# Performance work log

Hardware: AMD Instinct MI355X
Metric: run time of the kernel (lower is better)

## Reference

```python
import jax, jax.numpy as jnp
import numpy as np

EMBED_DIM = 1024
NUM_HEADS = 16
HEAD_DIM = EMBED_DIM // NUM_HEADS


def setup_inputs() -> dict:
    key = jax.random.key(0)
    ks = jax.random.split(key, 9)
    bs, seq_len = 4, 2048
    s = 1.0 / np.sqrt(EMBED_DIM)
    return {
        "x": jax.random.normal(ks[0], (bs, seq_len, EMBED_DIM), jnp.float32),
        "wq": jax.random.uniform(ks[1], (EMBED_DIM, EMBED_DIM), jnp.float32, -s, s),
        "bq": jax.random.uniform(ks[2], (EMBED_DIM,), jnp.float32, -s, s),
        "wk": jax.random.uniform(ks[3], (EMBED_DIM, EMBED_DIM), jnp.float32, -s, s),
        "bk": jax.random.uniform(ks[4], (EMBED_DIM,), jnp.float32, -s, s),
        "wv": jax.random.uniform(ks[5], (EMBED_DIM, EMBED_DIM), jnp.float32, -s, s),
        "bv": jax.random.uniform(ks[6], (EMBED_DIM,), jnp.float32, -s, s),
        "wo": jax.random.uniform(ks[7], (EMBED_DIM, EMBED_DIM), jnp.float32, -s, s),
        "bo": jax.random.uniform(ks[8], (EMBED_DIM,), jnp.float32, -s, s),
    }


def reference(x, wq, bq, wk, bk, wv, bv, wo, bo):
    bs, seq_len, _ = x.shape
    # projections (torch Linear: y = x @ W.T + b; here w stored as [out,in])
    q = x @ wq.T + bq
    k = x @ wk.T + bk
    v = x @ wv.T + bv
    # split heads -> (bs, heads, seq, head_dim)
    def split(t):
        return t.reshape(bs, seq_len, NUM_HEADS, HEAD_DIM).transpose(0, 2, 1, 3)
    q, k, v = split(q), split(k), split(v)
    scale = 1.0 / jnp.sqrt(jnp.asarray(HEAD_DIM, jnp.float32))
    scores = jnp.einsum("bhqd,bhkd->bhqk", q, k) * scale
    attn = jax.nn.softmax(scores, axis=-1)
    out = jnp.einsum("bhqk,bhkd->bhqd", attn, v)
    out = out.transpose(0, 2, 1, 3).reshape(bs, seq_len, EMBED_DIM)
    return out @ wo.T + bo
```

## Files before the change

kernel.cpp:

```cpp
#include <hip/hip_runtime.h>
#include <stdint.h>

#define SEQ 2048
#define BSZ 4
#define NH 16
#define HD 64
#define EMB 1024
#define NT (SEQ / 64)
#define QSCALE 0.1803368801111f

using bf16x8 = __attribute__((ext_vector_type(8))) __bf16;
using u16x8  = __attribute__((ext_vector_type(8))) unsigned short;
using u32x4  = __attribute__((ext_vector_type(4))) uint32_t;
using f32x4  = __attribute__((ext_vector_type(4))) float;
using f32x16 = __attribute__((ext_vector_type(16))) float;

__device__ __forceinline__ float exp2v(float x) { return __builtin_amdgcn_exp2f(x); }

__device__ __forceinline__ unsigned short f2bf(float f) {
    union { float f; uint32_t u; } v; v.f = f;
    uint32_t r = v.u + 0x7fffu + ((v.u >> 16) & 1u);
    return (unsigned short)(r >> 16);
}

__device__ __forceinline__ uint32_t cvtpk(float lo, float hi) {
    uint32_t r;
    asm("v_cvt_pk_bf16_f32 %0, %1, %2" : "=v"(r) : "v"(lo), "v"(hi));
    return r;
}
__device__ __forceinline__ void plswap(uint32_t& a, uint32_t& b) {
    asm volatile("v_permlane32_swap_b32 %0, %1" : "+v"(a), "+v"(b));
}

__device__ __forceinline__ void gload16(void* lds, const void* g) {
    __builtin_amdgcn_global_load_lds(
        (const __attribute__((address_space(1))) void*)g,
        (__attribute__((address_space(3))) void*)lds, 16, 0, 0);
}

__global__ void cast_kernel(const float* __restrict__ s, unsigned short* __restrict__ d, int n) {
    int i = (blockIdx.x * blockDim.x + threadIdx.x) * 4;
    if (i + 3 >= n) {
        for (int j = 0; j < 4 && i + j < n; ++j) d[i + j] = f2bf(s[i + j]);
        return;
    }
    float4 v = *(const float4*)(s + i);
    ushort4 o;
    o.x = f2bf(v.x); o.y = f2bf(v.y); o.z = f2bf(v.z); o.w = f2bf(v.w);
    *(ushort4*)(d + i) = o;
}

template <int MODE>
__global__ __launch_bounds__(256, 2)
void gemm_bt(const unsigned short* __restrict__ A,
             const unsigned short* __restrict__ Bw,
             const float* __restrict__ b0, const float* __restrict__ b1,
             const float* __restrict__ b2,
             void* __restrict__ C0, void* __restrict__ C1, void* __restrict__ C2,
             int M, int N, int Kd) {
    __shared__ unsigned short As[128][64];
    __shared__ unsigned short Bs[128][64];

    const int t    = threadIdx.x;
    const int lane = t & 63;
    const int wid  = t >> 6;
    const int g    = lane >> 4;
    const int lr   = lane & 15;
    const int wm   = wid >> 1, wn = wid & 1;
    const int m0   = blockIdx.x * 128, n0 = blockIdx.y * 128;
    const int srow = lane >> 3;
    const int scol = (lane & 7) * 8;

    f32x4 acc[4][4];
    const f32x4 zero = {0.f, 0.f, 0.f, 0.f};
#pragma unroll
    for (int i = 0; i < 4; ++i)
#pragma unroll
        for (int j = 0; j < 4; ++j) acc[i][j] = zero;

    for (int kt = 0; kt < Kd; kt += 64) {
#pragma unroll
        for (int p = 0; p < 4; ++p) {
            int rowA = wid * 32 + p * 8;
            gload16(&As[rowA][0], A  + (size_t)(m0 + rowA + srow) * Kd + kt + scol);
            gload16(&Bs[rowA][0], Bw + (size_t)(n0 + rowA + srow) * Kd + kt + scol);
        }
        __syncthreads();
#pragma unroll
        for (int ks = 0; ks < 2; ++ks) {
            bf16x8 af[4], bfr[4];
#pragma unroll
            for (int m = 0; m < 4; ++m)
                af[m] = *(const bf16x8*)&As[wm * 64 + m * 16 + lr][ks * 32 + g * 8];
#pragma unroll
            for (int n = 0; n < 4; ++n)
                bfr[n] = *(const bf16x8*)&Bs[wn * 64 + n * 16 + lr][ks * 32 + g * 8];
#pragma unroll
            for (int m = 0; m < 4; ++m)
#pragma unroll
                for (int n = 0; n < 4; ++n)
                    acc[m][n] = __builtin_amdgcn_mfma_f32_16x16x32_bf16(af[m], bfr[n], acc[m][n], 0, 0, 0);
        }
        __syncthreads();
    }

    int seg = MODE == 2 ? (n0 >> 10) : 0;
    if (MODE == 2 && seg == 2) {
        unsigned short* CwT = (unsigned short*)C2;
        int nl = n0 & 1023;
#pragma unroll
        for (int n = 0; n < 4; ++n) {
            int colL = nl + wn * 64 + n * 16 + lr;
            float bv = b2[colL];
#pragma unroll
            for (int m = 0; m < 4; ++m) {
                int rowg = m0 + wm * 64 + m * 16 + g * 4;
                int bb = rowg >> 11, seq = rowg & 2047;
                ushort4 w;
                w.x = f2bf(acc[m][n][0] + bv);
                w.y = f2bf(acc[m][n][1] + bv);
                w.z = f2bf(acc[m][n][2] + bv);
                w.w = f2bf(acc[m][n][3] + bv);
                *(ushort4*)(CwT + ((size_t)(bb * 1024 + colL)) * SEQ + seq) = w;
            }
        }
        return;
    }

    const float* bias;
    unsigned short* Cw = nullptr;
    float* Cf = nullptr;
    float scl = 1.0f;
    int nl;
    if (MODE == 2) {
        bias = seg == 0 ? b0 : b1;
        Cw = (unsigned short*)(seg == 0 ? C0 : C1);
        scl = seg == 0 ? QSCALE : 1.0f;
        nl = n0 & 1023;
    } else {
        bias = b0; Cf = (float*)C0; nl = n0;
    }
#pragma unroll
    for (int n = 0; n < 4; ++n) {
        int colL = nl + wn * 64 + n * 16 + lr;
        float bv = bias[colL];
#pragma unroll
        for (int m = 0; m < 4; ++m) {
            int rowg = m0 + wm * 64 + m * 16 + g * 4;
#pragma unroll
            for (int r = 0; r < 4; ++r) {
                float val = (acc[m][n][r] + bv) * scl;
                if (MODE == 2)
                    Cw[(size_t)(rowg + r) * EMB + colL] = f2bf(val);
                else
                    Cf[(size_t)(rowg + r) * EMB + colL] = val;
            }
        }
    }
}

__global__ __launch_bounds__(512, 4)
void flash_attn(const unsigned short* __restrict__ Q,
                const unsigned short* __restrict__ K,
                const unsigned short* __restrict__ VT,
                unsigned short* __restrict__ O) {
    __shared__ unsigned char KsB[2][64 * 128];
    __shared__ unsigned char VtB[2][64 * 128];

    const int nwg  = gridDim.x * gridDim.y * gridDim.z;
    const int cpx  = nwg >> 3;
    const int bid0 = (blockIdx.z * gridDim.y + blockIdx.y) * gridDim.x + blockIdx.x;
    const int bid  = (bid0 % 8) * cpx + (bid0 / 8);
    const int bx   = bid & (gridDim.x - 1);
    const int h    = (bid >> 3) & 15;
    const int b    = bid >> 7;

    const int t    = threadIdx.x;
    const int wid  = t >> 6;
    const int lane = t & 63;
    const int l31  = lane & 31;
    const int hi   = lane >> 5;
    const int hi16 = hi << 4;
    const int sw   = (l31 & 7) << 4;
    const int qbase = bx * 256 + wid * 32;
    const size_t rowbase = (size_t)b * SEQ;
    const unsigned short* Kh  = K + rowbase * EMB + h * HD;
    const unsigned short* Vth = VT + (size_t)(b * 1024 + h * HD) * SEQ;

    const int grow = t >> 3;
    const int gc16 = (t & 7) ^ (grow & 7);
    const unsigned short* Ksrc0 = Kh  + (size_t)grow * EMB + gc16 * 8;
    const unsigned short* Vsrc0 = Vth + (size_t)grow * SEQ + gc16 * 8;

    bf16x8 qf[4];
#pragma unroll
    for (int db = 0; db < 4; ++db)
        qf[db] = *(const bf16x8*)(Q + (rowbase + qbase + l31) * EMB + h * HD + db * 16 + hi * 8);

    bf16x8 vones;
#pragma unroll
    for (int j = 0; j < 8; ++j) vones[j] = (__bf16)1.0f;

    f32x16 o0, o1, o2;
#pragma unroll
    for (int r = 0; r < 16; ++r) { o0[r] = 0.f; o1[r] = 0.f; o2[r] = 0.f; }
    float me = -1e30f;

    auto issue_tile = [&](int kt) {
        unsigned char* Ks = KsB[kt & 1] + wid * 1024;
        unsigned char* Vt = VtB[kt & 1] + wid * 1024;
        gload16(Ks, Ksrc0 + (size_t)kt * 64 * EMB);
        gload16(Vt, Vsrc0 + kt * 64);
    };
    issue_tile(0);

    for (int kt = 0; kt < NT; ++kt) {
        unsigned char* Ks = KsB[kt & 1];
        unsigned char* Vt = VtB[kt & 1];

        __syncthreads();

        if (kt + 1 < NT) issue_tile(kt + 1);

        f32x16 s0, s1;
#pragma unroll
        for (int r = 0; r < 16; ++r) { s0[r] = 0.f; s1[r] = 0.f; }
        __builtin_amdgcn_s_setprio(1);
#pragma unroll
        for (int db = 0; db < 4; ++db) {
            bf16x8 kf0 = *(const bf16x8*)(Ks + l31 * 128        + ((db * 32 + hi16) ^ sw));
            bf16x8 kf1 = *(const bf16x8*)(Ks + (l31 + 32) * 128 + ((db * 32 + hi16) ^ sw));
            s0 = __builtin_amdgcn_mfma_f32_32x32x16_bf16(kf0, qf[db], s0, 0, 0, 0);
            s1 = __builtin_amdgcn_mfma_f32_32x32x16_bf16(kf1, qf[db], s1, 0, 0, 0);
        }
        __builtin_amdgcn_s_setprio(0);

        float pm = fmaxf(fmaxf(s0[0], s0[1]), s0[2]);
#pragma unroll
        for (int r = 3; r < 15; r += 2) pm = fmaxf(fmaxf(pm, s0[r]), s0[r + 1]);
        pm = fmaxf(pm, s0[15]);
#pragma unroll
        for (int r = 0; r < 16; r += 2) pm = fmaxf(fmaxf(pm, s1[r]), s1[r + 1]);
        pm = fmaxf(pm, __shfl_xor(pm, 32));

        if (!__all(pm - me <= 8.0f)) {
            float mn = fmaxf(me, pm);
            float al = exp2v(me - mn);
            me = mn;
#pragma unroll
            for (int r = 0; r < 16; ++r) {
                int addr = hi16 + (((r & 3) + 8 * (r >> 2)) << 2);
                float ar = __int_as_float(
                    __builtin_amdgcn_ds_bpermute(addr, __float_as_int(al)));
                o0[r] *= ar; o1[r] *= ar; o2[r] *= ar;
            }
        }

        s0 = s0 - me;
        s1 = s1 - me;
#pragma unroll
        for (int r = 0; r < 16; ++r) s0[r] = exp2v(s0[r]);
#pragma unroll
        for (int r = 0; r < 16; ++r) s1[r] = exp2v(s1[r]);

        bf16x8 pa[4];
#pragma unroll
        for (int kb = 0; kb < 2; ++kb) {
            uint32_t dw[8];
#pragma unroll
            for (int i = 0; i < 8; ++i)
                dw[i] = kb == 0 ? cvtpk(s0[2 * i], s0[2 * i + 1])
                                : cvtpk(s1[2 * i], s1[2 * i + 1]);
            plswap(dw[0], dw[2]); plswap(dw[1], dw[3]);
            plswap(dw[4], dw[6]); plswap(dw[5], dw[7]);
            u32x4 w0 = {dw[0], dw[1], dw[2], dw[3]};
            u32x4 w1 = {dw[4], dw[5], dw[6], dw[7]};
            pa[kb * 2]     = __builtin_bit_cast(bf16x8, w0);
            pa[kb * 2 + 1] = __builtin_bit_cast(bf16x8, w1);
        }

        __builtin_amdgcn_s_setprio(1);
#pragma unroll
        for (int kk = 0; kk < 4; ++kk) {
            bf16x8 vf0 = *(const bf16x8*)(Vt + l31 * 128        + ((kk * 32 + hi16) ^ sw));
            bf16x8 vf1 = *(const bf16x8*)(Vt + (l31 + 32) * 128 + ((kk * 32 + hi16) ^ sw));
            o0 = __builtin_amdgcn_mfma_f32_32x32x16_bf16(pa[kk], vf0, o0, 0, 0, 0);
            o1 = __builtin_amdgcn_mfma_f32_32x32x16_bf16(pa[kk], vf1, o1, 0, 0, 0);
            o2 = __builtin_amdgcn_mfma_f32_32x32x16_bf16(pa[kk], vones, o2, 0, 0, 0);
        }
        __builtin_amdgcn_s_setprio(0);
    }

#pragma unroll
    for (int r = 0; r < 16; ++r) {
        float inv = 1.0f / o2[r];
        int q = qbase + (r & 3) + 8 * (r >> 2) + 4 * hi;
        size_t ro = (rowbase + q) * EMB + h * HD;
        O[ro + l31]      = f2bf(o0[r] * inv);
        O[ro + 32 + l31] = f2bf(o1[r] * inv);
    }
}

extern "C" void kernel_launch(void* const* d_in, const int* in_sizes, int n_in,
                              void* d_out, int out_size, void* d_ws, size_t ws_size,
                              hipStream_t stream) {
    const float* x  = (const float*)d_in[0];
    const float* wq = (const float*)d_in[1];
    const float* bq = (const float*)d_in[2];
    const float* wk = (const float*)d_in[3];
    const float* bk = (const float*)d_in[4];
    const float* wv = (const float*)d_in[5];
    const float* bv = (const float*)d_in[6];
    const float* wo = (const float*)d_in[7];
    const float* bo = (const float*)d_in[8];

    char* ws = (char*)d_ws;
    const size_t M = (size_t)BSZ * SEQ;
    unsigned short* xb    = (unsigned short*)ws;
    unsigned short* wqkvb = (unsigned short*)(ws + (size_t)16 * 1024 * 1024);
    unsigned short* wob   = (unsigned short*)(ws + (size_t)22 * 1024 * 1024);
    unsigned short* Qb    = (unsigned short*)(ws + (size_t)24 * 1024 * 1024);
    unsigned short* Kb    = Qb + M * EMB;
    unsigned short* VTb   = Kb + M * EMB;

    const int nX = (int)(M * EMB);
    cast_kernel<<<nX / 1024, 256, 0, stream>>>(x, xb, nX);
    cast_kernel<<<1024, 256, 0, stream>>>(wq, wqkvb,                 EMB * EMB);
    cast_kernel<<<1024, 256, 0, stream>>>(wk, wqkvb + 1024 * 1024,   EMB * EMB);
    cast_kernel<<<1024, 256, 0, stream>>>(wv, wqkvb + 2 * 1024 * 1024, EMB * EMB);
    cast_kernel<<<1024, 256, 0, stream>>>(wo, wob, EMB * EMB);

    gemm_bt<2><<<dim3(64, 24), 256, 0, stream>>>(xb, wqkvb, bq, bk, bv,
                                                 Qb, Kb, VTb, (int)M, 3 * EMB, EMB);

    flash_attn<<<dim3(SEQ / 256, NH, BSZ), 512, 0, stream>>>(Qb, Kb, VTb, xb);

    gemm_bt<0><<<dim3(64, 8), 256, 0, stream>>>(xb, wob, bo, nullptr, nullptr,
                                                d_out, nullptr, nullptr, (int)M, EMB, EMB);
}
```

Before: 204.6 us.

## Software-pipeline flash attention QK and PV with triple buffering; merge weight casts

Restructures the flash attention loop so the QK^T MFMAs for tile kt are issued alongside the PV MFMAs for tile kt-1, with softmax packing afterwards. K/V LDS buffers go from double to triple buffering to hold the extra in-flight tile. This is meant to hide softmax latency behind matrix work. It also merges the four weight cast launches into one kernel using blockIdx.y to cut launch overhead, at the cost of more LDS per block, which could lower occupancy.

New measurement: 203.6 us. About the same (-0.5%).

```diff
diff --git a/kernel.cpp b/kernel.cpp
--- a/kernel.cpp
+++ b/kernel.cpp
@@ -44,6 +44,24 @@
         for (int j = 0; j < 4 && i + j < n; ++j) d[i + j] = f2bf(s[i + j]);
         return;
     }
+    float4 v = *(const float4*)(s + i);
+    ushort4 o;
+    o.x = f2bf(v.x); o.y = f2bf(v.y); o.z = f2bf(v.z); o.w = f2bf(v.w);
+    *(ushort4*)(d + i) = o;
+}
+
+__global__ void cast4_kernel(const float* __restrict__ w0, const float* __restrict__ w1,
+                             const float* __restrict__ w2, const float* __restrict__ w3,
+                             unsigned short* __restrict__ d0, unsigned short* __restrict__ d1,
+                             unsigned short* __restrict__ d2, unsigned short* __restrict__ d3) {
+    const float* s; unsigned short* d;
+    switch (blockIdx.y) {
+        case 0:  s = w0; d = d0; break;
+        case 1:  s = w1; d = d1; break;
+        case 2:  s = w2; d = d2; break;
+        default: s = w3; d = d3; break;
+    }
+    int i = (blockIdx.x * blockDim.x + threadIdx.x) * 4;
     float4 v = *(const float4*)(s + i);
     ushort4 o;
     o.x = f2bf(v.x); o.y = f2bf(v.y); o.z = f2bf(v.z); o.w = f2bf(v.w);
@@ -164,8 +182,8 @@
                 const unsigned short* __restrict__ K,
                 const unsigned short* __restrict__ VT,
                 unsigned short* __restrict__ O) {
-    __shared__ unsigned char KsB[2][64 * 128];
-    __shared__ unsigned char VtB[2][64 * 128];
+    __shared__ unsigned char KsB[3][64 * 128];
+    __shared__ unsigned char VtB[3][64 * 128];
 
     const int nwg  = gridDim.x * gridDim.y * gridDim.z;
     const int cpx  = nwg >> 3;
@@ -206,23 +224,12 @@
     for (int r = 0; r < 16; ++r) { o0[r] = 0.f; o1[r] = 0.f; o2[r] = 0.f; }
     float me = -1e30f;
 
-    auto issue_tile = [&](int kt) {
-        unsigned char* Ks = KsB[kt & 1] + wid * 1024;
-        unsigned char* Vt = VtB[kt & 1] + wid * 1024;
-        gload16(Ks, Ksrc0 + (size_t)kt * 64 * EMB);
-        gload16(Vt, Vsrc0 + kt * 64);
+    auto issue_tile = [&](int kt, int buf) {
+        gload16(KsB[buf] + wid * 1024, Ksrc0 + (size_t)kt * 64 * EMB);
+        gload16(VtB[buf] + wid * 1024, Vsrc0 + kt * 64);
     };
-    issue_tile(0);
-
-    for (int kt = 0; kt < NT; ++kt) {
-        unsigned char* Ks = KsB[kt & 1];
-        unsigned char* Vt = VtB[kt & 1];
-
-        __syncthreads();
-
-        if (kt + 1 < NT) issue_tile(kt + 1);
-
-        f32x16 s0, s1;
+
+    auto qk = [&](const unsigned char* Ks, f32x16& s0, f32x16& s1) {
 #pragma unroll
         for (int r = 0; r < 16; ++r) { s0[r] = 0.f; s1[r] = 0.f; }
         __builtin_amdgcn_s_setprio(1);
@@ -234,7 +241,22 @@
             s1 = __builtin_amdgcn_mfma_f32_32x32x16_bf16(kf1, qf[db], s1, 0, 0, 0);
         }
         __builtin_amdgcn_s_setprio(0);
-
+    };
+
+    auto pv = [&](const unsigned char* Vt, const bf16x8* pa) {
+        __builtin_amdgcn_s_setprio(1);
+#pragma unroll
+        for (int kk = 0; kk < 4; ++kk) {
+            bf16x8 vf0 = *(const bf16x8*)(Vt + l31 * 128        + ((kk * 32 + hi16) ^ sw));
+            bf16x8 vf1 = *(const bf16x8*)(Vt + (l31 + 32) * 128 + ((kk * 32 + hi16) ^ sw));
+            o0 = __builtin_amdgcn_mfma_f32_32x32x16_bf16(pa[kk], vf0, o0, 0, 0, 0);
+            o1 = __builtin_amdgcn_mfma_f32_32x32x16_bf16(pa[kk], vf1, o1, 0, 0, 0);
+            o2 = __builtin_amdgcn_mfma_f32_32x32x16_bf16(pa[kk], vones, o2, 0, 0, 0);
+        }
+        __builtin_amdgcn_s_setprio(0);
+    };
+
+    auto softmax_pack = [&](f32x16& s0, f32x16& s1, bf16x8* pa, bool first) {
         float pm = fmaxf(fmaxf(s0[0], s0[1]), s0[2]);
 #pragma unroll
         for (int r = 3; r < 15; r += 2) pm = fmaxf(fmaxf(pm, s0[r]), s0[r + 1]);
@@ -243,7 +265,9 @@
         for (int r = 0; r < 16; r += 2) pm = fmaxf(fmaxf(pm, s1[r]), s1[r + 1]);
         pm = fmaxf(pm, __shfl_xor(pm, 32));
 
-        if (!__all(pm - me <= 8.0f)) {
+        if (first) {
+            me = pm;
+        } else if (!__all(pm - me <= 8.0f)) {
             float mn = fmaxf(me, pm);
             float al = exp2v(me - mn);
             me = mn;
@@ -263,7 +287,6 @@
 #pragma unroll
         for (int r = 0; r < 16; ++r) s1[r] = exp2v(s1[r]);
 
-        bf16x8 pa[4];
 #pragma unroll
         for (int kb = 0; kb < 2; ++kb) {
             uint32_t dw[8];
@@ -278,18 +301,29 @@
             pa[kb * 2]     = __builtin_bit_cast(bf16x8, w0);
             pa[kb * 2 + 1] = __builtin_bit_cast(bf16x8, w1);
         }
-
-        __builtin_amdgcn_s_setprio(1);
-#pragma unroll
-        for (int kk = 0; kk < 4; ++kk) {
-            bf16x8 vf0 = *(const bf16x8*)(Vt + l31 * 128        + ((kk * 32 + hi16) ^ sw));
-            bf16x8 vf1 = *(const bf16x8*)(Vt + (l31 + 32) * 128 + ((kk * 32 + hi16) ^ sw));
-            o0 = __builtin_amdgcn_mfma_f32_32x32x16_bf16(pa[kk], vf0, o0, 0, 0, 0);
-            o1 = __builtin_amdgcn_mfma_f32_32x32x16_bf16(pa[kk], vf1, o1, 0, 0, 0);
-            o2 = __builtin_amdgcn_mfma_f32_32x32x16_bf16(pa[kk], vones, o2, 0, 0, 0);
-        }
-        __builtin_amdgcn_s_setprio(0);
-    }
+    };
+
+    issue_tile(0, 0);
+    __syncthreads();
+    issue_tile(1, 1);
+    bf16x8 paA[4];
+    {
+        f32x16 s0, s1;
+        qk(KsB[0], s0, s1);
+        softmax_pack(s0, s1, paA, true);
+    }
+
+    int prv = 0, cur = 1, nxt = 2;
+    for (int kt = 1; kt < NT; ++kt) {
+        __syncthreads();
+        if (kt + 1 < NT) issue_tile(kt + 1, nxt);
+        f32x16 s0, s1;
+        qk(KsB[cur], s0, s1);
+        pv(VtB[prv], paA);
+        softmax_pack(s0, s1, paA, false);
+        int tmp = prv; prv = cur; cur = nxt; nxt = tmp;
+    }
+    pv(VtB[prv], paA);
 
 #pragma unroll
     for (int r = 0; r < 16; ++r) {
@@ -325,10 +359,9 @@
 
     const int nX = (int)(M * EMB);
     cast_kernel<<<nX / 1024, 256, 0, stream>>>(x, xb, nX);
-    cast_kernel<<<1024, 256, 0, stream>>>(wq, wqkvb,                 EMB * EMB);
-    cast_kernel<<<1024, 256, 0, stream>>>(wk, wqkvb + 1024 * 1024,   EMB * EMB);
-    cast_kernel<<<1024, 256, 0, stream>>>(wv, wqkvb + 2 * 1024 * 1024, EMB * EMB);
-    cast_kernel<<<1024, 256, 0, stream>>>(wo, wob, EMB * EMB);
+    cast4_kernel<<<dim3(1024, 4), 256, 0, stream>>>(
+        wq, wk, wv, wo,
+        wqkvb, wqkvb + 1024 * 1024, wqkvb + 2 * 1024 * 1024, wob);
 
     gemm_bt<2><<<dim3(64, 24), 256, 0, stream>>>(xb, wqkvb, bq, bk, bv,
                                                  Qb, Kb, VTb, (int)M, 3 * EMB, EMB);
```

## Process two query sub-tiles per wave in flash attention and merge weight casts

Applied to the files above, without the earlier changes.

Each wave in the flash attention kernel now handles 64 query rows as two 32-row sub-tiles. It reuses the K fragments loaded from LDS and the V fragments across both, while the block drops from 512 to 256 threads. The goal is fewer LDS reads per MFMA and less barrier overhead per unit of work, at the cost of more registers, since there are now six accumulators and two sets of Q fragments, which may lower occupancy. Separately, the four weight-cast launches are merged into one kernel that uses a 2D grid to cut launch overhead.

Measured after the change: 231.7 us. 1.13x slower.

```diff
diff --git a/kernel.cpp b/kernel.cpp
--- a/kernel.cpp
+++ b/kernel.cpp
@@ -44,6 +44,24 @@
         for (int j = 0; j < 4 && i + j < n; ++j) d[i + j] = f2bf(s[i + j]);
         return;
     }
+    float4 v = *(const float4*)(s + i);
+    ushort4 o;
+    o.x = f2bf(v.x); o.y = f2bf(v.y); o.z = f2bf(v.z); o.w = f2bf(v.w);
+    *(ushort4*)(d + i) = o;
+}
+
+__global__ void cast4_kernel(const float* __restrict__ w0, const float* __restrict__ w1,
+                             const float* __restrict__ w2, const float* __restrict__ w3,
+                             unsigned short* __restrict__ d0, unsigned short* __restrict__ d1,
+                             unsigned short* __restrict__ d2, unsigned short* __restrict__ d3) {
+    const float* s; unsigned short* d;
+    switch (blockIdx.y) {
+        case 0:  s = w0; d = d0; break;
+        case 1:  s = w1; d = d1; break;
+        case 2:  s = w2; d = d2; break;
+        default: s = w3; d = d3; break;
+    }
+    int i = (blockIdx.x * blockDim.x + threadIdx.x) * 4;
     float4 v = *(const float4*)(s + i);
     ushort4 o;
     o.x = f2bf(v.x); o.y = f2bf(v.y); o.z = f2bf(v.z); o.w = f2bf(v.w);
@@ -159,7 +177,7 @@
     }
 }
 
-__global__ __launch_bounds__(512, 4)
+__global__ __launch_bounds__(256, 2)
 void flash_attn(const unsigned short* __restrict__ Q,
                 const unsigned short* __restrict__ K,
                 const unsigned short* __restrict__ VT,
@@ -182,59 +200,46 @@
     const int hi   = lane >> 5;
     const int hi16 = hi << 4;
     const int sw   = (l31 & 7) << 4;
-    const int qbase = bx * 256 + wid * 32;
+    const int qb0  = bx * 256 + wid * 64;
     const size_t rowbase = (size_t)b * SEQ;
     const unsigned short* Kh  = K + rowbase * EMB + h * HD;
     const unsigned short* Vth = VT + (size_t)(b * 1024 + h * HD) * SEQ;
 
-    const int grow = t >> 3;
-    const int gc16 = (t & 7) ^ (grow & 7);
-    const unsigned short* Ksrc0 = Kh  + (size_t)grow * EMB + gc16 * 8;
-    const unsigned short* Vsrc0 = Vth + (size_t)grow * SEQ + gc16 * 8;
-
-    bf16x8 qf[4];
-#pragma unroll
-    for (int db = 0; db < 4; ++db)
-        qf[db] = *(const bf16x8*)(Q + (rowbase + qbase + l31) * EMB + h * HD + db * 16 + hi * 8);
+    bf16x8 qf[2][4];
+#pragma unroll
+    for (int qs = 0; qs < 2; ++qs)
+#pragma unroll
+        for (int db = 0; db < 4; ++db)
+            qf[qs][db] = *(const bf16x8*)(Q + (rowbase + qb0 + qs * 32 + l31) * EMB
+                                            + h * HD + db * 16 + hi * 8);
 
     bf16x8 vones;
 #pragma unroll
     for (int j = 0; j < 8; ++j) vones[j] = (__bf16)1.0f;
 
-    f32x16 o0, o1, o2;
-#pragma unroll
-    for (int r = 0; r < 16; ++r) { o0[r] = 0.f; o1[r] = 0.f; o2[r] = 0.f; }
-    float me = -1e30f;
+    f32x16 oA0, oA1, oA2, oB0, oB1, oB2;
+#pragma unroll
+    for (int r = 0; r < 16; ++r) {
+        oA0[r] = 0.f; oA1[r] = 0.f; oA2[r] = 0.f;
+        oB0[r] = 0.f; oB1[r] = 0.f; oB2[r] = 0.f;
+    }
+    float meA = -1e30f, meB = -1e30f;
 
     auto issue_tile = [&](int kt) {
-        unsigned char* Ks = KsB[kt & 1] + wid * 1024;
-        unsigned char* Vt = VtB[kt & 1] + wid * 1024;
-        gload16(Ks, Ksrc0 + (size_t)kt * 64 * EMB);
-        gload16(Vt, Vsrc0 + kt * 64);
+#pragma unroll
+        for (int c = 0; c < 2; ++c) {
+            int slot = (wid * 2 + c) * 64 + lane;
+            int row  = slot >> 3;
+            int c16  = (slot & 7) ^ (row & 7);
+            gload16(KsB[kt & 1] + (wid * 2 + c) * 1024,
+                    Kh + (size_t)(kt * 64 + row) * EMB + c16 * 8);
+            gload16(VtB[kt & 1] + (wid * 2 + c) * 1024,
+                    Vth + (size_t)row * SEQ + (size_t)kt * 64 + c16 * 8);
+        }
     };
-    issue_tile(0);
-
-    for (int kt = 0; kt < NT; ++kt) {
-        unsigned char* Ks = KsB[kt & 1];
-        unsigned char* Vt = VtB[kt & 1];
-
-        __syncthreads();
-
-        if (kt + 1 < NT) issue_tile(kt + 1);
-
-        f32x16 s0, s1;
-#pragma unroll
-        for (int r = 0; r < 16; ++r) { s0[r] = 0.f; s1[r] = 0.f; }
-        __builtin_amdgcn_s_setprio(1);
-#pragma unroll
-        for (int db = 0; db < 4; ++db) {
-            bf16x8 kf0 = *(const bf16x8*)(Ks + l31 * 128        + ((db * 32 + hi16) ^ sw));
-            bf16x8 kf1 = *(const bf16x8*)(Ks + (l31 + 32) * 128 + ((db * 32 + hi16) ^ sw));
-            s0 = __builtin_amdgcn_mfma_f32_32x32x16_bf16(kf0, qf[db], s0, 0, 0, 0);
-            s1 = __builtin_amdgcn_mfma_f32_32x32x16_bf16(kf1, qf[db], s1, 0, 0, 0);
-        }
-        __builtin_amdgcn_s_setprio(0);
-
+
+    auto softmax_pack = [&](f32x16& s0, f32x16& s1, float& me,
+                            f32x16& o0, f32x16& o1, f32x16& o2, bf16x8* pa) {
         float pm = fmaxf(fmaxf(s0[0], s0[1]), s0[2]);
 #pragma unroll
         for (int r = 3; r < 15; r += 2) pm = fmaxf(fmaxf(pm, s0[r]), s0[r + 1]);
@@ -255,15 +260,12 @@
                 o0[r] *= ar; o1[r] *= ar; o2[r] *= ar;
             }
         }
-
         s0 = s0 - me;
         s1 = s1 - me;
 #pragma unroll
         for (int r = 0; r < 16; ++r) s0[r] = exp2v(s0[r]);
 #pragma unroll
         for (int r = 0; r < 16; ++r) s1[r] = exp2v(s1[r]);
-
-        bf16x8 pa[4];
 #pragma unroll
         for (int kb = 0; kb < 2; ++kb) {
             uint32_t dw[8];
@@ -278,26 +280,82 @@
             pa[kb * 2]     = __builtin_bit_cast(bf16x8, w0);
             pa[kb * 2 + 1] = __builtin_bit_cast(bf16x8, w1);
         }
+    };
+
+    issue_tile(0);
+
+    for (int kt = 0; kt < NT; ++kt) {
+        unsigned char* Ks = KsB[kt & 1];
+        unsigned char* Vt = VtB[kt & 1];
+
+        __syncthreads();
+        if (kt + 1 < NT) issue_tile(kt + 1);
+
+        bf16x8 kf[2][4];
+#pragma unroll
+        for (int db = 0; db < 4; ++db) {
+            kf[0][db] = *(const bf16x8*)(Ks + l31 * 128        + ((db * 32 + hi16) ^ sw));
+            kf[1][db] = *(const bf16x8*)(Ks + (l31 + 32) * 128 + ((db * 32 + hi16) ^ sw));
+        }
+
+        bf16x8 paA[4], paB[4];
+        {
+            f32x16 s0, s1;
+#pragma unroll
+            for (int r = 0; r < 16; ++r) { s0[r] = 0.f; s1[r] = 0.f; }
+            __builtin_amdgcn_s_setprio(1);
+#pragma unroll
+            for (int db = 0; db < 4; ++db) {
+                s0 = __builtin_amdgcn_mfma_f32_32x32x16_bf16(kf[0][db], qf[0][db], s0, 0, 0, 0);
+                s1 = __builtin_amdgcn_mfma_f32_32x32x16_bf16(kf[1][db], qf[0][db], s1, 0, 0, 0);
+            }
+            __builtin_amdgcn_s_setprio(0);
+            softmax_pack(s0, s1, meA, oA0, oA1, oA2, paA);
+        }
+        {
+            f32x16 s0, s1;
+#pragma unroll
+            for (int r = 0; r < 16; ++r) { s0[r] = 0.f; s1[r] = 0.f; }
+            __builtin_amdgcn_s_setprio(1);
+#pragma unroll
+            for (int db = 0; db < 4; ++db) {
+                s0 = __builtin_amdgcn_mfma_f32_32x32x16_bf16(kf[0][db], qf[1][db], s0, 0, 0, 0);
+                s1 = __builtin_amdgcn_mfma_f32_32x32x16_bf16(kf[1][db], qf[1][db], s1, 0, 0, 0);
+            }
+            __builtin_amdgcn_s_setprio(0);
+            softmax_pack(s0, s1, meB, oB0, oB1, oB2, paB);
+        }
 
         __builtin_amdgcn_s_setprio(1);
 #pragma unroll
         for (int kk = 0; kk < 4; ++kk) {
             bf16x8 vf0 = *(const bf16x8*)(Vt + l31 * 128        + ((kk * 32 + hi16) ^ sw));
             bf16x8 vf1 = *(const bf16x8*)(Vt + (l31 + 32) * 128 + ((kk * 32 + hi16) ^ sw));
-            o0 = __builtin_amdgcn_mfma_f32_32x32x16_bf16(pa[kk], vf0, o0, 0, 0, 0);
-            o1 = __builtin_amdgcn_mfma_f32_32x32x16_bf16(pa[kk], vf1, o1, 0, 0, 0);
-            o2 = __builtin_amdgcn_mfma_f32_32x32x16_bf16(pa[kk], vones, o2, 0, 0, 0);
+            oA0 = __builtin_amdgcn_mfma_f32_32x32x16_bf16(paA[kk], vf0, oA0, 0, 0, 0);
+            oA1 = __builtin_amdgcn_mfma_f32_32x32x16_bf16(paA[kk], vf1, oA1, 0, 0, 0);
+            oA2 = __builtin_amdgcn_mfma_f32_32x32x16_bf16(paA[kk], vones, oA2, 0, 0, 0);
+            oB0 = __builtin_amdgcn_mfma_f32_32x32x16_bf16(paB[kk], vf0, oB0, 0, 0, 0);
+            oB1 = __builtin_amdgcn_mfma_f32_32x32x16_bf16(paB[kk], vf1, oB1, 0, 0, 0);
+            oB2 = __builtin_amdgcn_mfma_f32_32x32x16_bf16(paB[kk], vones, oB2, 0, 0, 0);
         }
         __builtin_amdgcn_s_setprio(0);
     }
 
 #pragma unroll
     for (int r = 0; r < 16; ++r) {
-        float inv = 1.0f / o2[r];
-        int q = qbase + (r & 3) + 8 * (r >> 2) + 4 * hi;
-        size_t ro = (rowbase + q) * EMB + h * HD;
-        O[ro + l31]      = f2bf(o0[r] * inv);
-        O[ro + 32 + l31] = f2bf(o1[r] * inv);
+        int qoff = (r & 3) + 8 * (r >> 2) + 4 * hi;
+        {
+            float inv = 1.0f / oA2[r];
+            size_t ro = (rowbase + qb0 + qoff) * EMB + h * HD;
+            O[ro + l31]      = f2bf(oA0[r] * inv);
+            O[ro + 32 + l31] = f2bf(oA1[r] * inv);
+        }
+        {
+            float inv = 1.0f / oB2[r];
+            size_t ro = (rowbase + qb0 + 32 + qoff) * EMB + h * HD;
+            O[ro + l31]      = f2bf(oB0[r] * inv);
+            O[ro + 32 + l31] = f2bf(oB1[r] * inv);
+        }
     }
 }
 
@@ -325,15 +383,14 @@
 
     const int nX = (int)(M * EMB);
     cast_kernel<<<nX / 1024, 256, 0, stream>>>(x, xb, nX);
-    cast_kernel<<<1024, 256, 0, stream>>>(wq, wqkvb,                 EMB * EMB);
-    cast_kernel<<<1024, 256, 0, stream>>>(wk, wqkvb + 1024 * 1024,   EMB * EMB);
-    cast_kernel<<<1024, 256, 0, stream>>>(wv, wqkvb + 2 * 1024 * 1024, EMB * EMB);
-    cast_kernel<<<1024, 256, 0, stream>>>(wo, wob, EMB * EMB);
+    cast4_kernel<<<dim3(1024, 4), 256, 0, stream>>>(
+        wq, wk, wv, wo,
+        wqkvb, wqkvb + 1024 * 1024, wqkvb + 2 * 1024 * 1024, wob);
 
     gemm_bt<2><<<dim3(64, 24), 256, 0, stream>>>(xb, wqkvb, bq, bk, bv,
                                                  Qb, Kb, VTb, (int)M, 3 * EMB, EMB);
 
-    flash_attn<<<dim3(SEQ / 256, NH, BSZ), 512, 0, stream>>>(Qb, Kb, VTb, xb);
+    flash_attn<<<dim3(SEQ / 256, NH, BSZ), 256, 0, stream>>>(Qb, Kb, VTb, xb);
 
     gemm_bt<0><<<dim3(64, 8), 256, 0, stream>>>(xb, wob, bo, nullptr, nullptr,
                                                 d_out, nullptr, nullptr, (int)M, EMB, EMB);
```
